# Performance work log

Measured on AMD Instinct MI355X. Metric: run time of the kernel, lower is better.

## Reference

```python
import jax, jax.numpy as jnp
import numpy as np

N = 100_000      # nodes
E = 3_200_000    # edges
R = 5            # relations
B = 2            # bases
IN_F = 4
HID = 32


def setup_inputs() -> dict:
    key = jax.random.key(0)
    ks = jax.random.split(key, 24)
    # node features: one-hot hop/type labels; label 0 -> user node, label 1 -> item node
    node_ids = jnp.arange(N)
    x = jnp.eye(IN_F, dtype=jnp.float32)[node_ids % IN_F]
    src = jax.random.randint(ks[0], (E,), 0, N, dtype=jnp.int32)
    dst = jax.random.randint(ks[1], (E,), 0, N, dtype=jnp.int32)
    etype = jax.random.randint(ks[2], (E,), 0, R, dtype=jnp.int32)
    user_ids = jnp.arange(0, N, IN_F, dtype=jnp.int32)  # label==0 nodes
    item_ids = jnp.arange(1, N, IN_F, dtype=jnp.int32)  # label==1 nodes

    def p(k, shape, scale=0.1):
        return (jax.random.normal(k, shape, dtype=jnp.float32) * scale)

    inp = dict(x=x, src=src, dst=dst, etype=etype,
               user_ids=user_ids, item_ids=item_ids)
    dims = [IN_F, HID, HID, HID, HID]
    ki = 3
    for l in range(4):
        inp[f'bases{l}'] = p(ks[ki], (B, dims[l], dims[l + 1])); ki += 1
        inp[f'comp{l}'] = p(ks[ki], (R, B)); ki += 1
        inp[f'loop{l}'] = p(ks[ki], (dims[l], dims[l + 1])); ki += 1
        inp[f'b{l}'] = jnp.zeros((dims[l + 1],), jnp.float32)
    inp['w1'] = p(ks[ki], (2 * 4 * HID, 128)); ki += 1
    inp['bl1'] = jnp.zeros((128,), jnp.float32)
    inp['w2'] = p(ks[ki], (128, 1)); ki += 1
    inp['bl2'] = jnp.zeros((1,), jnp.float32)
    return inp


def _rgcn_layer(x, src, dst, etype, bases, comp, loopw, bias):
    # basis decomposition: W[r] = sum_b comp[r,b] * bases[b]
    W = jnp.einsum('rb,bio->rio', comp, bases)           # [R, in, out]
    xr = jnp.einsum('ni,rio->rno', x, W)                 # [R, N, out] (R,N small)
    msg = xr[etype, src]                                 # [E, out] gather
    agg = jax.ops.segment_sum(msg, dst, num_segments=x.shape[0])  # scatter-add
    return jnp.tanh(agg + x @ loopw + bias)


def reference(x, src, dst, etype, user_ids, item_ids,
              bases0, comp0, loop0, b0,
              bases1, comp1, loop1, b1,
              bases2, comp2, loop2, b2,
              bases3, comp3, loop3, b3,
              w1, bl1, w2, bl2):
    layers = [(bases0, comp0, loop0, b0), (bases1, comp1, loop1, b1),
              (bases2, comp2, loop2, b2), (bases3, comp3, loop3, b3)]
    h = x
    states = []
    for (ba, co, lo, bi) in layers:
        h = _rgcn_layer(h, src, dst, etype, ba, co, lo, bi)
        states.append(h)
    concat = jnp.concatenate(states, axis=1)             # [N, 128]
    g = jnp.concatenate([concat[user_ids], concat[item_ids]], axis=1)  # [G, 256]
    g = jax.nn.relu(g @ w1 + bl1)
    out = (g @ w2 + bl2)[:, 0]
    return out
```

## Files before the change

### kernel.cpp

```cpp
#include <hip/hip_runtime.h>
#include <hip/hip_fp16.h>

#define HID 32
#define R 5
#define BSH 8
#define BCAP 10240

__device__ __forceinline__ float fast_tanh(float x) {
    x = fminf(15.f, fmaxf(-15.f, x));
    float e = __expf(2.f * x);
    return (e - 1.f) / (e + 1.f);
}


__global__ void cursor_init(int* __restrict__ cursor, int K) {
    int i = blockIdx.x * blockDim.x + threadIdx.x;
    if (i < K) cursor[i] = i * BCAP;
}

__global__ void bucketB(const int* __restrict__ src, const int* __restrict__ dst,
                        const int* __restrict__ etype, int* __restrict__ cursor,
                        int* __restrict__ tmp, int E) {
    __shared__ int hist[512];
    __shared__ int sc[512];
    __shared__ int off[512];
    __shared__ int stag[8192];
    __shared__ unsigned short sb[8192];
    int tid = threadIdx.x;
    hist[tid] = 0;
    __syncthreads();
    int base = blockIdx.x * 8192;
    int tot = E - base;
    if (tot > 8192) tot = 8192;
    int lrank[16], pk[16], bk[16];
#pragma unroll
    for (int k = 0; k < 16; k++) {
        int e = base + k * 512 + tid;
        if (e < E) {
            int d = dst[e];
            int b = d >> BSH;
            bk[k] = b;
            pk[k] = src[e] | (etype[e] << 17) | ((d & 255) << 20);
            lrank[k] = atomicAdd(&hist[b], 1);
        } else {
            bk[k] = -1;
        }
    }
    __syncthreads();
    int v = hist[tid];
    sc[tid] = v;
    __syncthreads();
    for (int o = 1; o < 512; o <<= 1) {
        int t = 0;
        if (tid >= o) t = sc[tid - o];
        __syncthreads();
        if (tid >= o) sc[tid] += t;
        __syncthreads();
    }
    int excl = sc[tid] - v;
    off[tid] = excl;
    int gb = 0;
    if (v) gb = atomicAdd(&cursor[tid], v);
    __syncthreads();
    hist[tid] = gb - excl;
    __syncthreads();
#pragma unroll
    for (int k = 0; k < 16; k++) {
        if (bk[k] >= 0) {
            int s = off[bk[k]] + lrank[k];
            stag[s] = pk[k];
            sb[s] = (unsigned short)bk[k];
        }
    }
    __syncthreads();
    for (int s = tid; s < tot; s += 512) {
        int b = sb[s];
        tmp[s + hist[b]] = stag[s];
    }
}

__global__ void bucketC(const int* __restrict__ cursor, const int* __restrict__ tmp,
                        int* __restrict__ es, int* __restrict__ row_beg,
                        int* __restrict__ row_end, int N, int K) {
    __shared__ int hist[256];
    __shared__ int sc[256];
    __shared__ int cur[256];
    __shared__ int sorted[BCAP];
    int b = blockIdx.x;
    int tid = threadIdx.x;
    int beg = b * BCAP;
    int cnt = cursor[b] - beg;
    hist[tid] = 0;
    __syncthreads();
    for (int i = tid; i < cnt; i += 256)
        atomicAdd(&hist[tmp[beg + i] >> 20], 1);
    __syncthreads();
    int v = hist[tid];
    sc[tid] = v;
    __syncthreads();
    for (int o = 1; o < 256; o <<= 1) {
        int t = 0;
        if (tid >= o) t = sc[tid - o];
        __syncthreads();
        if (tid >= o) sc[tid] += t;
        __syncthreads();
    }
    int excl = sc[tid] - v;
    int d = (b << BSH) + tid;
    if (d < N) {
        row_beg[d] = beg + excl;
        row_end[d] = beg + excl + v;
    }
    cur[tid] = excl;
    __syncthreads();
    for (int i = tid; i < cnt; i += 256) {
        int p = tmp[beg + i];
        int pos = atomicAdd(&cur[p >> 20], 1);
        sorted[pos] = (p & 0x1FFFF) | (((p >> 17) & 7) << 20);
    }
    __syncthreads();
    for (int i = tid; i < cnt; i += 256)
        es[beg + i] = sorted[i];
}

__global__ void __launch_bounds__(256, 4)
agg0_kernel(const int* __restrict__ row_beg, const int* __restrict__ row_end,
            const int* __restrict__ es,
            const float* __restrict__ bases,
            const float* __restrict__ comp,
            const float* __restrict__ loopw,
            const float* __restrict__ bias,
            float* __restrict__ C, __half* __restrict__ xh_out, int N) {
    __shared__ float Wl[12 * 32];
    __shared__ float comp_l[12];
    __shared__ float S[128][13];
    int tid = threadIdx.x;
    if (tid < 12) comp_l[tid] = (tid < 10) ? comp[tid] : 0.f;
    for (int idx = tid; idx < 384; idx += 256) {
        int k = idx >> 5, c = idx & 31;
        Wl[idx] = (k < 8) ? bases[(k >> 2) * 128 + (k & 3) * 32 + c]
                          : loopw[(k - 8) * 32 + c];
    }
    __syncthreads();

    int g = tid >> 1, b = tid & 1;
    int d = blockIdx.x * 128 + g;
    bool valid = d < N;
    int beg = valid ? row_beg[d] : 0;
    int end = valid ? row_end[d] : 0;
    int cnt = end - beg;
    float4 acc = make_float4(0.f, 0.f, 0.f, 0.f);

    const int SENT = 5 << 20;
    int nbt = (cnt + 7) >> 3;
    for (int bb = 0; bb < nbt; bb++) {
        int p[8];
#pragma unroll
        for (int k = 0; k < 8; k++) {
            int j = bb * 8 + k;
            p[k] = (j < cnt) ? es[beg + j] : SENT;
        }
#pragma unroll
        for (int k = 0; k < 8; k++) {
            float c = comp_l[(p[k] >> 20) * 2 + b];
            int idx = p[k] & 3;
            acc.x += (idx == 0) ? c : 0.f;
            acc.y += (idx == 1) ? c : 0.f;
            acc.z += (idx == 2) ? c : 0.f;
            acc.w += (idx == 3) ? c : 0.f;
        }
    }
    S[g][b * 4 + 0] = acc.x;
    S[g][b * 4 + 1] = acc.y;
    S[g][b * 4 + 2] = acc.z;
    S[g][b * 4 + 3] = acc.w;
    if (b == 0) {
        int sel = d & 3;
        S[g][8]  = (valid && sel == 0) ? 1.f : 0.f;
        S[g][9]  = (valid && sel == 1) ? 1.f : 0.f;
        S[g][10] = (valid && sel == 2) ? 1.f : 0.f;
        S[g][11] = (valid && sel == 3) ? 1.f : 0.f;
    }
    __syncthreads();

    int c4 = tid & 7;
    float4 bi = *(const float4*)(bias + c4 * 4);
#pragma unroll
    for (int rr = 0; rr < 4; rr++) {
        int g2 = (tid >> 3) + 32 * rr;
        int d2 = blockIdx.x * 128 + g2;
        float4 o = bi;
#pragma unroll
        for (int k = 0; k < 12; k++) {
            float s = S[g2][k];
            float4 w = *(const float4*)&Wl[k * 32 + c4 * 4];
            o.x = fmaf(s, w.x, o.x);
            o.y = fmaf(s, w.y, o.y);
            o.z = fmaf(s, w.z, o.z);
            o.w = fmaf(s, w.w, o.w);
        }
        if (d2 < N) {
            float4 h;
            h.x = fast_tanh(o.x); h.y = fast_tanh(o.y);
            h.z = fast_tanh(o.z); h.w = fast_tanh(o.w);
            *(float4*)(C + (size_t)d2 * 128 + c4 * 4) = h;
            __half2 p0 = __floats2half2_rn(h.x, h.y);
            __half2 p1 = __floats2half2_rn(h.z, h.w);
            uint2 o2 = make_uint2(*(unsigned*)&p0, *(unsigned*)&p1);
            ((uint2*)(xh_out + (size_t)d2 * HID))[c4] = o2;
        }
    }
}

template<bool WRITE_XH>
__global__ void __launch_bounds__(256, 4)
agg_fused(const int* __restrict__ row_beg, const int* __restrict__ row_end,
          const int* __restrict__ es,
          const __half* __restrict__ xh_in,
          const float* __restrict__ bases,
          const float* __restrict__ comp,
          const float* __restrict__ loopw,
          const float* __restrict__ bias,
          float* __restrict__ C, __half* __restrict__ xh_out, int col_off, int N) {
    __shared__ float Wl[96 * 32];
    __shared__ float comp_l[12];
    __shared__ float S[32][97];
    int tid = threadIdx.x;
    if (tid < 12) comp_l[tid] = (tid < 10) ? comp[tid] : 0.f;
    for (int idx = tid; idx < 96 * 32; idx += 256)
        Wl[idx] = (idx < 2048) ? bases[idx] : loopw[idx - 2048];
    __syncthreads();

    int g = tid >> 3, c4 = tid & 7;
    int d = blockIdx.x * 32 + g;
    bool valid = d < N;
    int beg = valid ? row_beg[d] : 0;
    int end = valid ? row_end[d] : 0;
    int cnt = end - beg;
    float4 a0 = make_float4(0.f, 0.f, 0.f, 0.f);
    float4 a1 = make_float4(0.f, 0.f, 0.f, 0.f);

    const int SENT = 5 << 20;
    int nbt = (cnt + 7) >> 3;
    if (nbt > 0) {
        int p[8], pn[8];
#pragma unroll
        for (int k = 0; k < 8; k++) p[k] = (k < cnt) ? es[beg + k] : SENT;
        uint2 va[8];
#pragma unroll
        for (int k = 0; k < 8; k++)
            va[k] = ((const uint2*)(xh_in + (size_t)(p[k] & 0x1FFFF) * HID))[c4];
        if (nbt > 1) {
#pragma unroll
            for (int k = 0; k < 8; k++) {
                int j = 8 + k;
                pn[k] = (j < cnt) ? es[beg + j] : SENT;
            }
        }
        for (int bb = 1; bb < nbt; bb++) {
            int pt[8];
#pragma unroll
            for (int k = 0; k < 8; k++) pt[k] = pn[k];
            if (bb + 1 < nbt) {
#pragma unroll
                for (int k = 0; k < 8; k++) {
                    int j = (bb + 1) * 8 + k;
                    pn[k] = (j < cnt) ? es[beg + j] : SENT;
                }
            }
            uint2 vb[8];
#pragma unroll
            for (int k = 0; k < 8; k++)
                vb[k] = ((const uint2*)(xh_in + (size_t)(pt[k] & 0x1FFFF) * HID))[c4];
#pragma unroll
            for (int k = 0; k < 8; k++) {
                int et = p[k] >> 20;
                float c0 = comp_l[et * 2], c1 = comp_l[et * 2 + 1];
                float2 lo = __half22float2(*reinterpret_cast<__half2*>(&va[k].x));
                float2 hi = __half22float2(*reinterpret_cast<__half2*>(&va[k].y));
                a0.x = fmaf(c0, lo.x, a0.x); a1.x = fmaf(c1, lo.x, a1.x);
                a0.y = fmaf(c0, lo.y, a0.y); a1.y = fmaf(c1, lo.y, a1.y);
                a0.z = fmaf(c0, hi.x, a0.z); a1.z = fmaf(c1, hi.x, a1.z);
                a0.w = fmaf(c0, hi.y, a0.w); a1.w = fmaf(c1, hi.y, a1.w);
            }
#pragma unroll
            for (int k = 0; k < 8; k++) { va[k] = vb[k]; p[k] = pt[k]; }
        }
#pragma unroll
        for (int k = 0; k < 8; k++) {
            int et = p[k] >> 20;
            float c0 = comp_l[et * 2], c1 = comp_l[et * 2 + 1];
            float2 lo = __half22float2(*reinterpret_cast<__half2*>(&va[k].x));
            float2 hi = __half22float2(*reinterpret_cast<__half2*>(&va[k].y));
            a0.x = fmaf(c0, lo.x, a0.x); a1.x = fmaf(c1, lo.x, a1.x);
            a0.y = fmaf(c0, lo.y, a0.y); a1.y = fmaf(c1, lo.y, a1.y);
            a0.z = fmaf(c0, hi.x, a0.z); a1.z = fmaf(c1, hi.x, a1.z);
            a0.w = fmaf(c0, hi.y, a0.w); a1.w = fmaf(c1, hi.y, a1.w);
        }
    }
    *(float4*)&S[g][c4 * 4] = a0;
    *(float4*)&S[g][32 + c4 * 4] = a1;
    {
        uint2 vv = valid ? ((const uint2*)(xh_in + (size_t)d * HID))[c4]
                         : make_uint2(0u, 0u);
        float2 lo = __half22float2(*reinterpret_cast<__half2*>(&vv.x));
        float2 hi = __half22float2(*reinterpret_cast<__half2*>(&vv.y));
        S[g][64 + c4 * 4 + 0] = lo.x;
        S[g][64 + c4 * 4 + 1] = lo.y;
        S[g][64 + c4 * 4 + 2] = hi.x;
        S[g][64 + c4 * 4 + 3] = hi.y;
    }
    __syncthreads();

    float4 o = *(const float4*)(bias + c4 * 4);
#pragma unroll 8
    for (int k = 0; k < 96; k++) {
        float s = S[g][k];
        float4 w = *(const float4*)&Wl[k * 32 + c4 * 4];
        o.x = fmaf(s, w.x, o.x);
        o.y = fmaf(s, w.y, o.y);
        o.z = fmaf(s, w.z, o.z);
        o.w = fmaf(s, w.w, o.w);
    }
    if (valid) {
        float4 h;
        h.x = fast_tanh(o.x); h.y = fast_tanh(o.y);
        h.z = fast_tanh(o.z); h.w = fast_tanh(o.w);
        *(float4*)(C + (size_t)d * 128 + col_off + c4 * 4) = h;
        if (WRITE_XH) {
            __half2 p0 = __floats2half2_rn(h.x, h.y);
            __half2 p1 = __floats2half2_rn(h.z, h.w);
            uint2 o2 = make_uint2(*(unsigned*)&p0, *(unsigned*)&p1);
            ((uint2*)(xh_out + (size_t)d * HID))[c4] = o2;
        }
    }
}

#define MP 16
__global__ void __launch_bounds__(256, 4)
mlp_kernel(const float* __restrict__ C, const int* __restrict__ uid,
           const int* __restrict__ vid, const float* __restrict__ w1,
           const float* __restrict__ bl1, const float* __restrict__ w2,
           const float* __restrict__ bl2, float* __restrict__ out, int G) {
    __shared__ float feat[MP][2][128];
    __shared__ float psum[MP][128];
    int g0 = blockIdx.x * MP;
    int tid = threadIdx.x;

    for (int idx = tid; idx < MP * 64; idx += 256) {
        int g = idx >> 6;
        int rem = idx & 63;
        int which = rem >> 5;
        int q4 = rem & 31;
        int gg = g0 + g;
        float4 v = make_float4(0.f, 0.f, 0.f, 0.f);
        if (gg < G) {
            int node = which ? vid[gg] : uid[gg];
            v = ((const float4*)(C + (size_t)node * 128))[q4];
        }
        *(float4*)&feat[g][which][q4 * 4] = v;
    }
    __syncthreads();

    int q32 = tid & 31;
    int gs = (tid >> 5) & 3;
    int h = tid >> 7;
    float acc[4][4];
#pragma unroll
    for (int j = 0; j < 4; j++)
#pragma unroll
        for (int i = 0; i < 4; i++) acc[j][i] = 0.f;

    const float* wbase = w1 + (size_t)(h * 128) * 128 + q32 * 4;
    for (int k = 0; k < 128; k++) {
        float4 wv = *(const float4*)(wbase + (size_t)k * 128);
        float fv[4];
#pragma unroll
        for (int j = 0; j < 4; j++) fv[j] = feat[gs * 4 + j][h][k];
#pragma unroll
        for (int j = 0; j < 4; j++) {
            acc[j][0] = fmaf(fv[j], wv.x, acc[j][0]);
            acc[j][1] = fmaf(fv[j], wv.y, acc[j][1]);
            acc[j][2] = fmaf(fv[j], wv.z, acc[j][2]);
            acc[j][3] = fmaf(fv[j], wv.w, acc[j][3]);
        }
    }

    if (h == 1) {
#pragma unroll
        for (int j = 0; j < 4; j++)
#pragma unroll
            for (int i = 0; i < 4; i++)
                psum[gs * 4 + j][q32 * 4 + i] = acc[j][i];
    }
    __syncthreads();
    if (h == 0) {
#pragma unroll
        for (int j = 0; j < 4; j++) {
#pragma unroll
            for (int i = 0; i < 4; i++) {
                int q = q32 * 4 + i;
                float t = acc[j][i] + psum[gs * 4 + j][q] + bl1[q];
                psum[gs * 4 + j][q] = fmaxf(t, 0.f) * w2[q];
            }
        }
    }
    __syncthreads();

    float b2 = bl2[0];
#pragma unroll
    for (int pass = 0; pass < 2; pass++) {
        int g = (tid >> 5) + pass * 8;
        int l = tid & 31;
        float s = psum[g][l] + psum[g][l + 32] + psum[g][l + 64] + psum[g][l + 96];
        s += __shfl_down(s, 16, 32);
        s += __shfl_down(s, 8, 32);
        s += __shfl_down(s, 4, 32);
        s += __shfl_down(s, 2, 32);
        s += __shfl_down(s, 1, 32);
        if (l == 0 && g0 + g < G) out[g0 + g] = s + b2;
    }
}

extern "C" void kernel_launch(void* const* d_in, const int* in_sizes, int n_in,
                              void* d_out, int out_size, void* d_ws, size_t ws_size,
                              hipStream_t stream) {
    const int* src   = (const int*)d_in[1];
    const int* dst   = (const int*)d_in[2];
    const int* etype = (const int*)d_in[3];
    const int* uid   = (const int*)d_in[4];
    const int* vid   = (const int*)d_in[5];
    int N = in_sizes[0] / 4;
    int E = in_sizes[1];
    int G = in_sizes[4];
    int K = ((N + 255) >> BSH);

    char* wp = (char*)d_ws;
    auto alloc = [&](size_t bytes) {
        char* p = wp;
        wp += (bytes + 255) & ~(size_t)255;
        return p;
    };
    int* row_beg  = (int*)alloc((size_t)N * 4);
    int* row_end  = (int*)alloc((size_t)N * 4);
    int* cursor   = (int*)alloc(512 * 4);
    int* es       = (int*)alloc((size_t)K * BCAP * 4);
    __half* xhA   = (__half*)alloc((size_t)N * HID * 2);
    __half* xhB   = (__half*)alloc((size_t)N * HID * 2);
    float* C      = (float*)alloc((size_t)N * 128 * 4);
    int* tmp      = (int*)C;

    cursor_init<<<1, 512, 0, stream>>>(cursor, K);
    bucketB<<<(E + 8191) / 8192, 512, 0, stream>>>(src, dst, etype, cursor, tmp, E);
    bucketC<<<K, 256, 0, stream>>>(cursor, tmp, es, row_beg, row_end, N, K);

    agg0_kernel<<<(N + 127) / 128, 256, 0, stream>>>(
        row_beg, row_end, es,
        (const float*)d_in[6], (const float*)d_in[7],
        (const float*)d_in[8], (const float*)d_in[9],
        C, xhA, N);

    int ab = (N + 31) / 32;
    agg_fused<true><<<ab, 256, 0, stream>>>(
        row_beg, row_end, es, xhA,
        (const float*)d_in[10], (const float*)d_in[11],
        (const float*)d_in[12], (const float*)d_in[13],
        C, xhB, 32, N);
    agg_fused<true><<<ab, 256, 0, stream>>>(
        row_beg, row_end, es, xhB,
        (const float*)d_in[14], (const float*)d_in[15],
        (const float*)d_in[16], (const float*)d_in[17],
        C, xhA, 64, N);
    agg_fused<false><<<ab, 256, 0, stream>>>(
        row_beg, row_end, es, xhA,
        (const float*)d_in[18], (const float*)d_in[19],
        (const float*)d_in[20], (const float*)d_in[21],
        C, nullptr, 96, N);

    int gblocks = (G + MP - 1) / MP;
    mlp_kernel<<<gblocks, 256, 0, stream>>>(C, uid, vid,
                                            (const float*)d_in[22], (const float*)d_in[23],
                                            (const float*)d_in[24], (const float*)d_in[25],
                                            (float*)d_out, G);
}
```

Measured before the change: 373.4 us.

## Fuse layer-0 aggregation into bucket sort and store concat features in fp16

The first RGCN layer is computed inside the bucket-sort kernel straight from the shared-memory sorted edge list. This removes a separate launch and a re-read of the edge stream and row pointers. The concatenated per-layer activation buffer is now stored in half precision, halving its write and gather traffic for the MLP. In exchange the fused kernel uses more shared memory and does serial per-thread edge loops, and the MLP inputs lose some precision.

```diff
diff --git a/kernel.cpp b/kernel.cpp
--- a/kernel.cpp
+++ b/kernel.cpp
@@ -79,15 +79,30 @@
     }
 }
 
-__global__ void bucketC(const int* __restrict__ cursor, const int* __restrict__ tmp,
-                        int* __restrict__ es, int* __restrict__ row_beg,
-                        int* __restrict__ row_end, int N, int K) {
+__global__ void bucketC_agg0(const int* __restrict__ cursor, const int* __restrict__ tmp,
+                             int* __restrict__ es, int* __restrict__ row_beg,
+                             int* __restrict__ row_end,
+                             const float* __restrict__ bases,
+                             const float* __restrict__ comp,
+                             const float* __restrict__ loopw,
+                             const float* __restrict__ bias,
+                             __half* __restrict__ Ch, __half* __restrict__ xh_out,
+                             int N, int K) {
+    __shared__ int sorted[BCAP];
     __shared__ int hist[256];
     __shared__ int sc[256];
     __shared__ int cur[256];
-    __shared__ int sorted[BCAP];
+    __shared__ float Wl[12 * 32];
+    __shared__ float comp_l[12];
+    __shared__ float S[256][13];
     int b = blockIdx.x;
     int tid = threadIdx.x;
+    if (tid < 12) comp_l[tid] = (tid < 10) ? comp[tid] : 0.f;
+    for (int idx = tid; idx < 384; idx += 256) {
+        int k = idx >> 5, c = idx & 31;
+        Wl[idx] = (k < 8) ? bases[(k >> 2) * 128 + (k & 3) * 32 + c]
+                          : loopw[(k - 8) * 32 + c];
+    }
     int beg = b * BCAP;
     int cnt = cursor[b] - beg;
     hist[tid] = 0;
@@ -107,7 +122,8 @@
     }
     int excl = sc[tid] - v;
     int d = (b << BSH) + tid;
-    if (d < N) {
+    bool valid = d < N;
+    if (valid) {
         row_beg[d] = beg + excl;
         row_end[d] = beg + excl + v;
     }
@@ -121,74 +137,31 @@
     __syncthreads();
     for (int i = tid; i < cnt; i += 256)
         es[beg + i] = sorted[i];
-}
-
-__global__ void __launch_bounds__(256, 4)
-agg0_kernel(const int* __restrict__ row_beg, const int* __restrict__ row_end,
-            const int* __restrict__ es,
-            const float* __restrict__ bases,
-            const float* __restrict__ comp,
-            const float* __restrict__ loopw,
-            const float* __restrict__ bias,
-            float* __restrict__ C, __half* __restrict__ xh_out, int N) {
-    __shared__ float Wl[12 * 32];
-    __shared__ float comp_l[12];
-    __shared__ float S[128][13];
-    int tid = threadIdx.x;
-    if (tid < 12) comp_l[tid] = (tid < 10) ? comp[tid] : 0.f;
-    for (int idx = tid; idx < 384; idx += 256) {
-        int k = idx >> 5, c = idx & 31;
-        Wl[idx] = (k < 8) ? bases[(k >> 2) * 128 + (k & 3) * 32 + c]
-                          : loopw[(k - 8) * 32 + c];
-    }
-    __syncthreads();
-
-    int g = tid >> 1, b = tid & 1;
-    int d = blockIdx.x * 128 + g;
-    bool valid = d < N;
-    int beg = valid ? row_beg[d] : 0;
-    int end = valid ? row_end[d] : 0;
-    int cnt = end - beg;
-    float4 acc = make_float4(0.f, 0.f, 0.f, 0.f);
-
-    const int SENT = 5 << 20;
-    int nbt = (cnt + 7) >> 3;
-    for (int bb = 0; bb < nbt; bb++) {
-        int p[8];
-#pragma unroll
-        for (int k = 0; k < 8; k++) {
-            int j = bb * 8 + k;
-            p[k] = (j < cnt) ? es[beg + j] : SENT;
-        }
-#pragma unroll
-        for (int k = 0; k < 8; k++) {
-            float c = comp_l[(p[k] >> 20) * 2 + b];
-            int idx = p[k] & 3;
-            acc.x += (idx == 0) ? c : 0.f;
-            acc.y += (idx == 1) ? c : 0.f;
-            acc.z += (idx == 2) ? c : 0.f;
-            acc.w += (idx == 3) ? c : 0.f;
-        }
-    }
-    S[g][b * 4 + 0] = acc.x;
-    S[g][b * 4 + 1] = acc.y;
-    S[g][b * 4 + 2] = acc.z;
-    S[g][b * 4 + 3] = acc.w;
-    if (b == 0) {
+    float a0[4] = {0.f, 0.f, 0.f, 0.f};
+    float a1[4] = {0.f, 0.f, 0.f, 0.f};
+    for (int i = excl; i < excl + v; i++) {
+        int p = sorted[i];
+        int et = p >> 20;
+        int s3 = p & 3;
+        a0[s3] += comp_l[et * 2];
+        a1[s3] += comp_l[et * 2 + 1];
+    }
+#pragma unroll
+    for (int i = 0; i < 4; i++) { S[tid][i] = a0[i]; S[tid][4 + i] = a1[i]; }
+    {
         int sel = d & 3;
-        S[g][8]  = (valid && sel == 0) ? 1.f : 0.f;
-        S[g][9]  = (valid && sel == 1) ? 1.f : 0.f;
-        S[g][10] = (valid && sel == 2) ? 1.f : 0.f;
-        S[g][11] = (valid && sel == 3) ? 1.f : 0.f;
-    }
-    __syncthreads();
-
+        S[tid][8]  = (valid && sel == 0) ? 1.f : 0.f;
+        S[tid][9]  = (valid && sel == 1) ? 1.f : 0.f;
+        S[tid][10] = (valid && sel == 2) ? 1.f : 0.f;
+        S[tid][11] = (valid && sel == 3) ? 1.f : 0.f;
+    }
+    __syncthreads();
     int c4 = tid & 7;
     float4 bi = *(const float4*)(bias + c4 * 4);
 #pragma unroll
-    for (int rr = 0; rr < 4; rr++) {
+    for (int rr = 0; rr < 8; rr++) {
         int g2 = (tid >> 3) + 32 * rr;
-        int d2 = blockIdx.x * 128 + g2;
+        int d2 = (b << BSH) + g2;
         float4 o = bi;
 #pragma unroll
         for (int k = 0; k < 12; k++) {
@@ -200,13 +173,10 @@
             o.w = fmaf(s, w.w, o.w);
         }
         if (d2 < N) {
-            float4 h;
-            h.x = fast_tanh(o.x); h.y = fast_tanh(o.y);
-            h.z = fast_tanh(o.z); h.w = fast_tanh(o.w);
-            *(float4*)(C + (size_t)d2 * 128 + c4 * 4) = h;
-            __half2 p0 = __floats2half2_rn(h.x, h.y);
-            __half2 p1 = __floats2half2_rn(h.z, h.w);
+            __half2 p0 = __floats2half2_rn(fast_tanh(o.x), fast_tanh(o.y));
+            __half2 p1 = __floats2half2_rn(fast_tanh(o.z), fast_tanh(o.w));
             uint2 o2 = make_uint2(*(unsigned*)&p0, *(unsigned*)&p1);
+            ((uint2*)(Ch + (size_t)d2 * 128))[c4] = o2;
             ((uint2*)(xh_out + (size_t)d2 * HID))[c4] = o2;
         }
     }
@@ -221,7 +191,7 @@
           const float* __restrict__ comp,
           const float* __restrict__ loopw,
           const float* __restrict__ bias,
-          float* __restrict__ C, __half* __restrict__ xh_out, int col_off, int N) {
+          __half* __restrict__ Ch, __half* __restrict__ xh_out, int col_off, int N) {
     __shared__ float Wl[96 * 32];
     __shared__ float comp_l[12];
     __shared__ float S[32][97];
@@ -323,14 +293,11 @@
         o.w = fmaf(s, w.w, o.w);
     }
     if (valid) {
-        float4 h;
-        h.x = fast_tanh(o.x); h.y = fast_tanh(o.y);
-        h.z = fast_tanh(o.z); h.w = fast_tanh(o.w);
-        *(float4*)(C + (size_t)d * 128 + col_off + c4 * 4) = h;
+        __half2 p0 = __floats2half2_rn(fast_tanh(o.x), fast_tanh(o.y));
+        __half2 p1 = __floats2half2_rn(fast_tanh(o.z), fast_tanh(o.w));
+        uint2 o2 = make_uint2(*(unsigned*)&p0, *(unsigned*)&p1);
+        ((uint2*)(Ch + (size_t)d * 128 + col_off))[c4] = o2;
         if (WRITE_XH) {
-            __half2 p0 = __floats2half2_rn(h.x, h.y);
-            __half2 p1 = __floats2half2_rn(h.z, h.w);
-            uint2 o2 = make_uint2(*(unsigned*)&p0, *(unsigned*)&p1);
             ((uint2*)(xh_out + (size_t)d * HID))[c4] = o2;
         }
     }
@@ -338,7 +305,7 @@
 
 #define MP 16
 __global__ void __launch_bounds__(256, 4)
-mlp_kernel(const float* __restrict__ C, const int* __restrict__ uid,
+mlp_kernel(const __half* __restrict__ Ch, const int* __restrict__ uid,
            const int* __restrict__ vid, const float* __restrict__ w1,
            const float* __restrict__ bl1, const float* __restrict__ w2,
            const float* __restrict__ bl2, float* __restrict__ out, int G) {
@@ -353,12 +320,18 @@
         int which = rem >> 5;
         int q4 = rem & 31;
         int gg = g0 + g;
-        float4 v = make_float4(0.f, 0.f, 0.f, 0.f);
+        uint2 raw = make_uint2(0u, 0u);
         if (gg < G) {
             int node = which ? vid[gg] : uid[gg];
-            v = ((const float4*)(C + (size_t)node * 128))[q4];
-        }
-        *(float4*)&feat[g][which][q4 * 4] = v;
+            raw = ((const uint2*)(Ch + (size_t)node * 128 + which * 0))[q4 + which * 0];
+            raw = ((const uint2*)(Ch + (size_t)node * 128))[q4];
+        }
+        float2 f0 = __half22float2(*reinterpret_cast<__half2*>(&raw.x));
+        float2 f1 = __half22float2(*reinterpret_cast<__half2*>(&raw.y));
+        feat[g][which][q4 * 4 + 0] = f0.x;
+        feat[g][which][q4 * 4 + 1] = f0.y;
+        feat[g][which][q4 * 4 + 2] = f1.x;
+        feat[g][which][q4 * 4 + 3] = f1.y;
     }
     __syncthreads();
 
@@ -445,40 +418,37 @@
     int* row_end  = (int*)alloc((size_t)N * 4);
     int* cursor   = (int*)alloc(512 * 4);
     int* es       = (int*)alloc((size_t)K * BCAP * 4);
+    int* tmp      = (int*)alloc((size_t)K * BCAP * 4);
     __half* xhA   = (__half*)alloc((size_t)N * HID * 2);
     __half* xhB   = (__half*)alloc((size_t)N * HID * 2);
-    float* C      = (float*)alloc((size_t)N * 128 * 4);
-    int* tmp      = (int*)C;
+    __half* Ch    = (__half*)alloc((size_t)N * 128 * 2);
 
     cursor_init<<<1, 512, 0, stream>>>(cursor, K);
     bucketB<<<(E + 8191) / 8192, 512, 0, stream>>>(src, dst, etype, cursor, tmp, E);
-    bucketC<<<K, 256, 0, stream>>>(cursor, tmp, es, row_beg, row_end, N, K);
-
-    agg0_kernel<<<(N + 127) / 128, 256, 0, stream>>>(
-        row_beg, row_end, es,
-        (const float*)d_in[6], (const float*)d_in[7],
-        (const float*)d_in[8], (const float*)d_in[9],
-        C, xhA, N);
+    bucketC_agg0<<<K, 256, 0, stream>>>(cursor, tmp, es, row_beg, row_end,
+                                        (const float*)d_in[6], (const float*)d_in[7],
+                                        (const float*)d_in[8], (const float*)d_in[9],
+                                        Ch, xhA, N, K);
 
     int ab = (N + 31) / 32;
     agg_fused<true><<<ab, 256, 0, stream>>>(
         row_beg, row_end, es, xhA,
         (const float*)d_in[10], (const float*)d_in[11],
         (const float*)d_in[12], (const float*)d_in[13],
-        C, xhB, 32, N);
+        Ch, xhB, 32, N);
     agg_fused<true><<<ab, 256, 0, stream>>>(
         row_beg, row_end, es, xhB,
         (const float*)d_in[14], (const float*)d_in[15],
         (const float*)d_in[16], (const float*)d_in[17],
-        C, xhA, 64, N);
+        Ch, xhA, 64, N);
     agg_fused<false><<<ab, 256, 0, stream>>>(
         row_beg, row_end, es, xhA,
         (const float*)d_in[18], (const float*)d_in[19],
         (const float*)d_in[20], (const float*)d_in[21],
-        C, nullptr, 96, N);
+        Ch, nullptr, 96, N);
 
     int gblocks = (G + MP - 1) / MP;
-    mlp_kernel<<<gblocks, 256, 0, stream>>>(C, uid, vid,
+    mlp_kernel<<<gblocks, 256, 0, stream>>>(Ch, uid, vid,
                                             (const float*)d_in[22], (const float*)d_in[23],
                                             (const float*)d_in[24], (const float*)d_in[25],
                                             (float*)d_out, G);
```

New measurement: 360.4 us. 1.04x faster.
